# Kernel tuning notes

Hardware: AMD Instinct MI355X
Metric: run time of the kernel (lower is better)

The kernel has to match this reference:

```python
import jax, jax.numpy as jnp
import numpy as np

ROPE_THETA = 500000.0


def apply_rope(x, position_ids):
    # x: (B, H, S, hd), position_ids: (B, S)
    hd = x.shape[-1]
    inv_freq = 1.0 / (ROPE_THETA ** (jnp.arange(0, hd, 2, dtype=x.dtype) / hd))  # (hd/2,)
    freqs = position_ids.astype(x.dtype)[:, :, None] * inv_freq  # (B, S, hd/2)
    sin = jnp.sin(freqs)[:, None, :, :]  # (B, 1, S, hd/2)
    cos = jnp.cos(freqs)[:, None, :, :]
    x1 = x[..., ::2]
    x2 = x[..., 1::2]
    even = x1 * cos - x2 * sin
    odd = x2 * cos + x1 * sin
    # interleave even/odd back: stack on a new trailing axis then flatten
    return jnp.stack([even, odd], axis=-1).reshape(x.shape)


def setup_inputs() -> dict:
    key = jax.random.key(0)
    k_x, k_q, k_k, k_v, k_o = jax.random.split(key, 5)
    B, S, D = 2, 2048, 2048
    H, H_kv = 32, 8
    hd = D // H
    x = jax.random.normal(k_x, (B, S, D), dtype=jnp.float32)
    position_ids = jnp.broadcast_to(jnp.arange(S, dtype=jnp.int64)[None, :], (B, S))
    scale = 0.02
    Wq = jax.random.normal(k_q, (D, H * hd), dtype=jnp.float32) * scale
    Wk = jax.random.normal(k_k, (D, H_kv * hd), dtype=jnp.float32) * scale
    Wv = jax.random.normal(k_v, (D, H_kv * hd), dtype=jnp.float32) * scale
    Wo = jax.random.normal(k_o, (D, D), dtype=jnp.float32) * scale
    return {"x": x, "position_ids": position_ids, "Wq": Wq, "Wk": Wk, "Wv": Wv, "Wo": Wo}


def reference(x, position_ids, Wq, Wk, Wv, Wo):
    B, S, D = x.shape
    H, H_kv = 32, 8
    hd = D // H
    G = H // H_kv  # query heads per kv head

    q = (x @ Wq).reshape(B, S, H, hd).transpose(0, 2, 1, 3)        # (B, H, S, hd)
    k = (x @ Wk).reshape(B, S, H_kv, hd).transpose(0, 2, 1, 3)     # (B, H_kv, S, hd)
    v = (x @ Wv).reshape(B, S, H_kv, hd).transpose(0, 2, 1, 3)

    q = apply_rope(q, position_ids)
    k = apply_rope(k, position_ids)

    # GQA: group query heads (B, H_kv, G, S, hd); repeat_interleave maps head h -> kv head h // G
    qg = q.reshape(B, H_kv, G, S, hd)
    scores = jnp.einsum("bkgsh,bkth->bkgst", qg, k) / jnp.sqrt(jnp.asarray(hd, x.dtype))

    causal = jnp.triu(jnp.ones((S, S), dtype=bool), 1)  # True = masked
    scores = jnp.where(causal, jnp.asarray(-jnp.inf, scores.dtype), scores)

    attn = jax.nn.softmax(scores, axis=-1)  # (B, H_kv, G, S, S)
    z = jnp.einsum("bkgst,bkth->bkgsh", attn, v)  # (B, H_kv, G, S, hd)
    z = z.reshape(B, H, S, hd).transpose(0, 2, 1, 3).reshape(B, S, D)
    return z @ Wo
```

## Files before the change

### kernel.cpp

```cpp
#include <hip/hip_runtime.h>
#include <hip/hip_bf16.h>


#define S_LEN 2048
#define DIM   2048
#define NH    32
#define NKV   8
#define HD    64
#define BS    4096
#define NQKV  3072
#define LL(x) ((long long)(x))

typedef __bf16 bf16x8 __attribute__((ext_vector_type(8)));
typedef float  f32x4  __attribute__((ext_vector_type(4)));
typedef float  f32x16 __attribute__((ext_vector_type(16)));
typedef unsigned u32x4 __attribute__((ext_vector_type(4)));

__device__ __forceinline__ unsigned short bfb(float f) {
  __hip_bfloat16 h = __float2bfloat16(f);
  return *reinterpret_cast<unsigned short*>(&h);
}

__device__ __forceinline__ unsigned cvtpk(float lo, float hi) {
  unsigned u;
  asm("v_cvt_pk_bf16_f32 %0, %1, %2" : "=v"(u) : "v"(lo), "v"(hi));
  return u;
}

__device__ __forceinline__ void gload16(const void* g, void* l) {
  __builtin_amdgcn_global_load_lds(
      (const __attribute__((address_space(1))) void*)g,
      (__attribute__((address_space(3))) void*)l, 16, 0, 0);
}

__global__ void k_rope_tab(float* __restrict__ tab) {
  int i = blockIdx.x * 256 + threadIdx.x;
  if (i >= S_LEN * 32) return;
  int s = i >> 5, f = i & 31;
  double inv = pow(500000.0, -2.0 * (double)f / 64.0);
  double fr = (double)s * inv;
  tab[2 * i]     = (float)cos(fr);
  tab[2 * i + 1] = (float)sin(fr);
}

__global__ void k_cast4(const float* __restrict__ in, unsigned short* __restrict__ out, int n4) {
  int i = blockIdx.x * 256 + threadIdx.x;
  if (i >= n4) return;
  float4 v = ((const float4*)in)[i];
  ushort4 o;
  o.x = bfb(v.x); o.y = bfb(v.y); o.z = bfb(v.z); o.w = bfb(v.w);
  ((ushort4*)out)[i] = o;
}

__global__ void k_tcast(const float* __restrict__ in, unsigned short* __restrict__ out,
                        int K, int N) {
  __shared__ float tile[32][33];
  int n0 = blockIdx.x * 32, k0 = blockIdx.y * 32;
  int tx = threadIdx.x, ty = threadIdx.y;
#pragma unroll
  for (int r = 0; r < 32; r += 8) tile[ty + r][tx] = in[LL(k0 + ty + r) * N + n0 + tx];
  __syncthreads();
#pragma unroll
  for (int r = 0; r < 32; r += 8) out[LL(n0 + ty + r) * K + k0 + tx] = bfb(tile[tx][ty + r]);
}

__global__ void k_vtrans(const unsigned short* __restrict__ vbuf, unsigned short* __restrict__ vt) {
  __shared__ __align__(16) unsigned short tile[64][72];
  int s0 = blockIdx.x * 64;
  int bh = blockIdx.y;
  int b = bh >> 3, kvh = bh & 7;
  int t = threadIdx.x;
#pragma unroll
  for (int c = t; c < 512; c += 256) {
    int s = c >> 3, seg = c & 7;
    *(uint4*)&tile[s][seg * 8] =
        *(const uint4*)(vbuf + LL(b * S_LEN + s0 + s) * (NKV * HD) + kvh * HD + seg * 8);
  }
  __syncthreads();
#pragma unroll
  for (int c = t; c < 512; c += 256) {
    int d = c >> 3, sseg = c & 7;
    ushort4 x0, x1;
    unsigned short* xp = (unsigned short*)&x0;
#pragma unroll
    for (int j = 0; j < 4; j++) xp[j] = tile[sseg * 8 + j][d];
    unsigned short* yp = (unsigned short*)&x1;
#pragma unroll
    for (int j = 0; j < 4; j++) yp[j] = tile[sseg * 8 + 4 + j][d];
    uint4 o;
    o.x = ((unsigned*)&x0)[0]; o.y = ((unsigned*)&x0)[1];
    o.z = ((unsigned*)&x1)[0]; o.w = ((unsigned*)&x1)[1];
    *(uint4*)(vt + (LL(bh) * HD + d) * S_LEN + s0 + sseg * 8) = o;
  }
}

template <int MODE>
__global__ __launch_bounds__(256, 2) void k_gemm(
    const unsigned short* __restrict__ A, const unsigned short* __restrict__ Bt,
    void* __restrict__ Cout, int M, int N, int K,
    const float* __restrict__ tab, unsigned short* __restrict__ qbuf,
    unsigned short* __restrict__ kbuf, unsigned short* __restrict__ vbuf) {
  __shared__ __align__(16) unsigned short As[128 * 32];
  __shared__ __align__(16) unsigned short Bs[128 * 32];
  int t = threadIdx.x;
  int lane = t & 63, w = t >> 6;
  int wr = w >> 1, wc = w & 1;
  int g = lane >> 4, r = lane & 15;
  int gx = gridDim.x;
  int nwg = gx * gridDim.y;
  int lin = blockIdx.y * gx + blockIdx.x;
  int cpx = nwg >> 3;
  int swz = (lin & 7) * cpx + (lin >> 3);
  int bx = swz % gx, by = swz / gx;
  long long rowBase = LL(by) * 128;
  long long colBase = LL(bx) * 128;

  f32x4 acc[4][4] = {};

  int c0 = t, c1 = t + 256;
  const unsigned short* ag0 = A + (rowBase + (c0 >> 2)) * K + (c0 & 3) * 8;
  const unsigned short* ag1 = A + (rowBase + (c1 >> 2)) * K + (c1 & 3) * 8;
  const unsigned short* bg0 = Bt + (colBase + (c0 >> 2)) * K + (c0 & 3) * 8;
  const unsigned short* bg1 = Bt + (colBase + (c1 >> 2)) * K + (c1 & 3) * 8;
  char* lA0 = (char*)As + c0 * 16; char* lA1 = (char*)As + c1 * 16;
  char* lB0 = (char*)Bs + c0 * 16; char* lB1 = (char*)Bs + c1 * 16;

  for (int kt = 0; kt < K; kt += 32) {
    __syncthreads();
    gload16(ag0 + kt, lA0);
    gload16(ag1 + kt, lA1);
    gload16(bg0 + kt, lB0);
    gload16(bg1 + kt, lB1);
    __syncthreads();

    bf16x8 af[4], bfr[4];
#pragma unroll
    for (int m = 0; m < 4; m++)
      af[m] = *(const bf16x8*)(const void*)(As + (wr * 64 + m * 16 + r) * 32 + g * 8);
#pragma unroll
    for (int n = 0; n < 4; n++)
      bfr[n] = *(const bf16x8*)(const void*)(Bs + (wc * 64 + n * 16 + r) * 32 + g * 8);
#pragma unroll
    for (int m = 0; m < 4; m++)
#pragma unroll
      for (int n = 0; n < 4; n++)
        acc[m][n] = __builtin_amdgcn_mfma_f32_16x16x32_bf16(af[m], bfr[n], acc[m][n], 0, 0, 0);
  }

  if (MODE == 0) {
#pragma unroll
    for (int m = 0; m < 4; m++)
#pragma unroll
      for (int n = 0; n < 4; n++) {
        long long row0 = rowBase + wr * 64 + m * 16 + g * 4;
        long long col = colBase + wc * 64 + n * 16 + r;
#pragma unroll
        for (int j = 0; j < 4; j++)
          ((float*)Cout)[(row0 + j) * N + col] = acc[m][n][j];
      }
  } else {
#pragma unroll
    for (int n = 0; n < 4; n++) {
      int gc0 = (int)colBase + wc * 64 + n * 16;
      int gc = gc0 + r;
      unsigned short* dst; int dcol, dstride; float scale; bool rope;
      if (gc0 < 2048)      { dst = qbuf; dcol = gc;        dstride = DIM; scale = 0.18033688f; rope = true; }
      else if (gc0 < 2560) { dst = kbuf; dcol = gc - 2048; dstride = 512; scale = 1.0f;        rope = true; }
      else                 { dst = vbuf; dcol = gc - 2560; dstride = 512; scale = 1.0f;        rope = false; }
      int f = (gc & 63) >> 1;
      float sgn = (gc & 1) ? 1.f : -1.f;
#pragma unroll
      for (int m = 0; m < 4; m++) {
        long long row0 = rowBase + wr * 64 + m * 16 + g * 4;
#pragma unroll
        for (int j = 0; j < 4; j++) {
          float v = acc[m][n][j];
          float o;
          if (rope) {
            float part = __shfl_xor(v, 1);
            int s = (int)((row0 + j) & (S_LEN - 1));
            float cc = tab[(s * 32 + f) * 2], ss = tab[(s * 32 + f) * 2 + 1];
            o = (v * cc + sgn * part * ss) * scale;
          } else o = v;
          dst[(row0 + j) * dstride + dcol] = bfb(o);
        }
      }
    }
  }
}

__global__ __launch_bounds__(256, 2) void k_attn(
    const unsigned short* __restrict__ qb, const unsigned short* __restrict__ kb,
    const unsigned short* __restrict__ vt, unsigned short* __restrict__ zb) {
  int lin = blockIdx.x + 8 * (blockIdx.y + 32 * blockIdx.z);
  int kvh = lin & 7;
  int idx = lin >> 3;
  int b = idx >> 5;
  int j = idx & 31;
  int h = kvh * 4 + (j & 3);
  int pair = j >> 2;
  int bh = b * NKV + kvh;

  int t = threadIdx.x, lane = t & 63, w = t >> 6;
  int l31 = lane & 31, hi = lane >> 5;
  int sw = (l31 & 7) * 8;

  __shared__ __align__(16) unsigned short Ks[2][64 * 64];
  __shared__ __align__(16) unsigned short Vs[2][64 * 64];

  int c0 = t, c1 = t + 256;
  const unsigned short* kg0 = kb + LL(b) * S_LEN * 512 + (c0 >> 3) * 512 + kvh * HD
                                 + (((c0 & 7) ^ ((c0 >> 3) & 7)) * 8);
  const unsigned short* kg1 = kb + LL(b) * S_LEN * 512 + (c1 >> 3) * 512 + kvh * HD
                                 + (((c1 & 7) ^ ((c1 >> 3) & 7)) * 8);
  const unsigned short* vg0 = vt + (LL(bh) * HD + (c0 >> 3)) * S_LEN
                                 + (((c0 & 7) ^ ((c0 >> 3) & 7)) * 8);
  const unsigned short* vg1 = vt + (LL(bh) * HD + (c1 >> 3)) * S_LEN
                                 + (((c1 & 7) ^ ((c1 >> 3) & 7)) * 8);

#define STAGE(bufi, kst_)                                              \
  {                                                                    \
    gload16(kg0 + LL(kst_) * 512, (char*)Ks[bufi] + c0 * 16);          \
    gload16(kg1 + LL(kst_) * 512, (char*)Ks[bufi] + c1 * 16);          \
    gload16(vg0 + (kst_), (char*)Vs[bufi] + c0 * 16);                  \
    gload16(vg1 + (kst_), (char*)Vs[bufi] + c1 * 16);                  \
  }

#pragma unroll 1
  for (int pass = 0; pass < 2; pass++) {
    int st = pass ? (15 - pair) : pair;
    int rowb = st * 128 + w * 32;
    int qg = rowb + l31;
    long long qrow = LL(b) * S_LEN + qg;

    bf16x8 qf[4];
#pragma unroll
    for (int s = 0; s < 4; s++)
      qf[s] = *(const bf16x8*)(const void*)(qb + qrow * DIM + h * HD + s * 16 + hi * 8);

    f32x16 acc0 = {}, acc1 = {};
    float mrun = -1e30f, lrun = 0.f;

    int nt = 2 * st + 2;
    __syncthreads();
    STAGE(0, 0);
    for (int tt = 0; tt < nt; tt++) {
      int kst = tt * 64;
      int cur = tt & 1;
      if (tt + 1 < nt) {
        STAGE(cur ^ 1, kst + 64);
        asm volatile("s_waitcnt vmcnt(4)" ::: "memory");
      } else {
        asm volatile("s_waitcnt vmcnt(0)" ::: "memory");
      }
      __builtin_amdgcn_s_barrier();
      __builtin_amdgcn_sched_barrier(0);

      if (kst <= rowb + 31) {
        const unsigned short* Kc = Ks[cur];
        const unsigned short* Vc = Vs[cur];

        bf16x8 kf[2][4];
#pragma unroll
        for (int kbi = 0; kbi < 2; kbi++)
#pragma unroll
          for (int s = 0; s < 4; s++)
            kf[kbi][s] = *(const bf16x8*)(const void*)(
                Kc + (kbi * 32 + l31) * 64 + ((s * 16 + hi * 8) ^ sw));

        __builtin_amdgcn_s_setprio(1);
        f32x16 sc0 = {}, sc1 = {};
#pragma unroll
        for (int s = 0; s < 4; s++) {
          sc0 = __builtin_amdgcn_mfma_f32_32x32x16_bf16(kf[0][s], qf[s], sc0, 0, 0, 0);
          sc1 = __builtin_amdgcn_mfma_f32_32x32x16_bf16(kf[1][s], qf[s], sc1, 0, 0, 0);
        }
        __builtin_amdgcn_s_setprio(0);

        bf16x8 vf[8];
#pragma unroll
        for (int db = 0; db < 2; db++)
#pragma unroll
          for (int f = 0; f < 4; f++)
            vf[db * 4 + f] = *(const bf16x8*)(const void*)(
                Vc + (db * 32 + l31) * 64 + ((f * 16 + hi * 8) ^ sw));

        if (kst + 63 > rowb) {
#pragma unroll
          for (int q = 0; q < 16; q++) {
            int kl = (q & 3) + 8 * (q >> 2) + 4 * hi;
            if (kst + kl > qg) sc0[q] = -1e30f;
            if (kst + 32 + kl > qg) sc1[q] = -1e30f;
          }
        }

        float pm = -1e30f;
#pragma unroll
        for (int q = 0; q < 16; q++) {
          pm = fmaxf(pm, sc0[q]);
          pm = fmaxf(pm, sc1[q]);
        }
        pm = fmaxf(pm, __shfl_xor(pm, 32));
        if (__any(pm > mrun + 12.0f)) {
          float mnew = fmaxf(mrun, pm);
          float al = exp2f(mrun - mnew);
          mrun = mnew;
          lrun *= al;
          acc0 *= al;
          acc1 *= al;
        }
        f32x16 pv0, pv1;
        float ls = 0.f;
#pragma unroll
        for (int q = 0; q < 16; q++) {
          pv0[q] = exp2f(sc0[q] - mrun);
          pv1[q] = exp2f(sc1[q] - mrun);
          ls += pv0[q] + pv1[q];
        }
        lrun += ls + __shfl_xor(ls, 32);

        bf16x8 pfr[4];
#pragma unroll
        for (int f = 0; f < 4; f++) {
          int qb_ = (f & 1) * 8;
          float e0, e1, e2, e3, e4, e5, e6, e7;
          if (f < 2) {
            e0 = pv0[qb_ + 0]; e1 = pv0[qb_ + 1]; e2 = pv0[qb_ + 2]; e3 = pv0[qb_ + 3];
            e4 = pv0[qb_ + 4]; e5 = pv0[qb_ + 5]; e6 = pv0[qb_ + 6]; e7 = pv0[qb_ + 7];
          } else {
            e0 = pv1[qb_ + 0]; e1 = pv1[qb_ + 1]; e2 = pv1[qb_ + 2]; e3 = pv1[qb_ + 3];
            e4 = pv1[qb_ + 4]; e5 = pv1[qb_ + 5]; e6 = pv1[qb_ + 6]; e7 = pv1[qb_ + 7];
          }
          unsigned a0 = cvtpk(e0, e1), a1 = cvtpk(e2, e3);
          unsigned b0 = cvtpk(e4, e5), b1 = cvtpk(e6, e7);
          unsigned y0 = __shfl_xor(hi ? a0 : b0, 32);
          unsigned y1 = __shfl_xor(hi ? a1 : b1, 32);
          u32x4 uu;
          uu[0] = hi ? y0 : a0;
          uu[1] = hi ? y1 : a1;
          uu[2] = hi ? b0 : y0;
          uu[3] = hi ? b1 : y1;
          pfr[f] = *(bf16x8*)&uu;
        }

        __builtin_amdgcn_s_setprio(1);
#pragma unroll
        for (int f = 0; f < 4; f++) {
          acc0 = __builtin_amdgcn_mfma_f32_32x32x16_bf16(vf[f],     pfr[f], acc0, 0, 0, 0);
          acc1 = __builtin_amdgcn_mfma_f32_32x32x16_bf16(vf[4 + f], pfr[f], acc1, 0, 0, 0);
        }
        __builtin_amdgcn_s_setprio(0);
      }

      __builtin_amdgcn_sched_barrier(0);
      __builtin_amdgcn_s_barrier();
    }

    float invl = 1.0f / lrun;
#pragma unroll
    for (int q4 = 0; q4 < 4; q4++) {
      uint2 u;
      u.x = cvtpk(acc0[q4 * 4 + 0] * invl, acc0[q4 * 4 + 1] * invl);
      u.y = cvtpk(acc0[q4 * 4 + 2] * invl, acc0[q4 * 4 + 3] * invl);
      *(uint2*)(void*)(zb + qrow * DIM + h * HD + 8 * q4 + 4 * hi) = u;
      uint2 v;
      v.x = cvtpk(acc1[q4 * 4 + 0] * invl, acc1[q4 * 4 + 1] * invl);
      v.y = cvtpk(acc1[q4 * 4 + 2] * invl, acc1[q4 * 4 + 3] * invl);
      *(uint2*)(void*)(zb + qrow * DIM + h * HD + 32 + 8 * q4 + 4 * hi) = v;
    }
  }
#undef STAGE
}

extern "C" void kernel_launch(void* const* d_in, const int* in_sizes, int n_in,
                              void* d_out, int out_size, void* d_ws, size_t ws_size,
                              hipStream_t stream) {
  const float* x  = (const float*)d_in[0];
  const float* Wq = (const float*)d_in[2];
  const float* Wk = (const float*)d_in[3];
  const float* Wv = (const float*)d_in[4];
  const float* Wo = (const float*)d_in[5];
  float* out = (float*)d_out;

  char* wsb = (char*)d_ws;
  size_t off = 0;
  auto alloc = [&](size_t bytes) {
    void* p = wsb + off;
    off += (bytes + 255) & ~(size_t)255;
    return p;
  };
  float* tab            = (float*)alloc(LL(S_LEN) * 32 * 2 * 4);
  unsigned short* xb    = (unsigned short*)alloc(LL(BS) * DIM * 2);
  unsigned short* wqkvt = (unsigned short*)alloc(LL(NQKV) * DIM * 2);
  unsigned short* wot   = (unsigned short*)alloc(LL(DIM) * DIM * 2);
  unsigned short* qbuf  = (unsigned short*)alloc(LL(BS) * DIM * 2);
  unsigned short* kbuf  = (unsigned short*)alloc(LL(BS) * (NKV * HD) * 2);
  unsigned short* vbuf  = (unsigned short*)alloc(LL(BS) * (NKV * HD) * 2);
  unsigned short* vtb   = (unsigned short*)alloc(LL(2 * NKV) * HD * S_LEN * 2);
  unsigned short* zb    = (unsigned short*)alloc(LL(BS) * DIM * 2);

  k_rope_tab<<<(S_LEN * 32 + 255) / 256, 256, 0, stream>>>(tab);
  k_cast4<<<(BS * DIM / 4 + 255) / 256, 256, 0, stream>>>(x, xb, BS * DIM / 4);
  k_tcast<<<dim3(DIM / 32, DIM / 32), dim3(32, 8), 0, stream>>>(Wq, wqkvt, DIM, DIM);
  k_tcast<<<dim3(512 / 32, DIM / 32), dim3(32, 8), 0, stream>>>(Wk, wqkvt + LL(2048) * DIM, DIM, 512);
  k_tcast<<<dim3(512 / 32, DIM / 32), dim3(32, 8), 0, stream>>>(Wv, wqkvt + LL(2560) * DIM, DIM, 512);
  k_tcast<<<dim3(DIM / 32, DIM / 32), dim3(32, 8), 0, stream>>>(Wo, wot, DIM, DIM);

  k_gemm<2><<<dim3(NQKV / 128, BS / 128), 256, 0, stream>>>(
      xb, wqkvt, nullptr, BS, NQKV, DIM, tab, qbuf, kbuf, vbuf);

  k_vtrans<<<dim3(S_LEN / 64, 2 * NKV), 256, 0, stream>>>(vbuf, vtb);

  k_attn<<<dim3(8, NH, 2), 256, 0, stream>>>(qbuf, kbuf, vtb, zb);

  k_gemm<0><<<dim3(DIM / 128, BS / 128), 256, 0, stream>>>(
      zb, wot, out, BS, DIM, DIM, nullptr, nullptr, nullptr, nullptr);
}
```

Baseline: 229.8 us.

## Shrink attention blocks to two waves with 64-row query tiles

Attention blocks drop from 4 to 2 wavefronts, each covering 64 query rows, and the grid doubles so the causal work is split finer. Because every wave now needs every loaded KV tile, the per-tile skip check is removed and masking only runs on the last tile. The row max now uses v_max3 reductions and the row-sum cross-half shuffle moves out of the loop to the end. Each thread issues twice as many global-to-LDS loads per stage, and K/V tiles are reused across fewer waves, which raises load traffic per unit of compute.

```diff
diff --git a/kernel.cpp b/kernel.cpp
--- a/kernel.cpp
+++ b/kernel.cpp
@@ -25,6 +25,12 @@
   unsigned u;
   asm("v_cvt_pk_bf16_f32 %0, %1, %2" : "=v"(u) : "v"(lo), "v"(hi));
   return u;
+}
+
+__device__ __forceinline__ float fmax3(float a, float b, float c) {
+  float d;
+  asm("v_max3_f32 %0, %1, %2, %3" : "=v"(d) : "v"(a), "v"(b), "v"(c));
+  return d;
 }
 
 __device__ __forceinline__ void gload16(const void* g, void* l) {
@@ -189,14 +195,14 @@
   }
 }
 
-__global__ __launch_bounds__(256, 2) void k_attn(
+__global__ __launch_bounds__(128, 2) void k_attn(
     const unsigned short* __restrict__ qb, const unsigned short* __restrict__ kb,
     const unsigned short* __restrict__ vt, unsigned short* __restrict__ zb) {
-  int lin = blockIdx.x + 8 * (blockIdx.y + 32 * blockIdx.z);
+  int lin = blockIdx.x + 16 * (blockIdx.y + 32 * blockIdx.z);
   int kvh = lin & 7;
   int idx = lin >> 3;
-  int b = idx >> 5;
-  int j = idx & 31;
+  int b = idx >> 6;
+  int j = idx & 63;
   int h = kvh * 4 + (j & 3);
   int pair = j >> 2;
   int bh = b * NKV + kvh;
@@ -208,28 +214,34 @@
   __shared__ __align__(16) unsigned short Ks[2][64 * 64];
   __shared__ __align__(16) unsigned short Vs[2][64 * 64];
 
-  int c0 = t, c1 = t + 256;
-  const unsigned short* kg0 = kb + LL(b) * S_LEN * 512 + (c0 >> 3) * 512 + kvh * HD
-                                 + (((c0 & 7) ^ ((c0 >> 3) & 7)) * 8);
-  const unsigned short* kg1 = kb + LL(b) * S_LEN * 512 + (c1 >> 3) * 512 + kvh * HD
-                                 + (((c1 & 7) ^ ((c1 >> 3) & 7)) * 8);
-  const unsigned short* vg0 = vt + (LL(bh) * HD + (c0 >> 3)) * S_LEN
-                                 + (((c0 & 7) ^ ((c0 >> 3) & 7)) * 8);
-  const unsigned short* vg1 = vt + (LL(bh) * HD + (c1 >> 3)) * S_LEN
-                                 + (((c1 & 7) ^ ((c1 >> 3) & 7)) * 8);
+  int c0 = t, c1 = t + 128, c2 = t + 256, c3 = t + 384;
+#define KGP(c) (kb + LL(b) * S_LEN * 512 + ((c) >> 3) * 512 + kvh * HD \
+                   + ((((c) & 7) ^ (((c) >> 3) & 7)) * 8))
+#define VGP(c) (vt + (LL(bh) * HD + ((c) >> 3)) * S_LEN \
+                   + ((((c) & 7) ^ (((c) >> 3) & 7)) * 8))
+  const unsigned short* kg0 = KGP(c0); const unsigned short* kg1 = KGP(c1);
+  const unsigned short* kg2 = KGP(c2); const unsigned short* kg3 = KGP(c3);
+  const unsigned short* vg0 = VGP(c0); const unsigned short* vg1 = VGP(c1);
+  const unsigned short* vg2 = VGP(c2); const unsigned short* vg3 = VGP(c3);
+#undef KGP
+#undef VGP
 
 #define STAGE(bufi, kst_)                                              \
   {                                                                    \
     gload16(kg0 + LL(kst_) * 512, (char*)Ks[bufi] + c0 * 16);          \
     gload16(kg1 + LL(kst_) * 512, (char*)Ks[bufi] + c1 * 16);          \
+    gload16(kg2 + LL(kst_) * 512, (char*)Ks[bufi] + c2 * 16);          \
+    gload16(kg3 + LL(kst_) * 512, (char*)Ks[bufi] + c3 * 16);          \
     gload16(vg0 + (kst_), (char*)Vs[bufi] + c0 * 16);                  \
     gload16(vg1 + (kst_), (char*)Vs[bufi] + c1 * 16);                  \
+    gload16(vg2 + (kst_), (char*)Vs[bufi] + c2 * 16);                  \
+    gload16(vg3 + (kst_), (char*)Vs[bufi] + c3 * 16);                  \
   }
 
 #pragma unroll 1
   for (int pass = 0; pass < 2; pass++) {
-    int st = pass ? (15 - pair) : pair;
-    int rowb = st * 128 + w * 32;
+    int st = pass ? (31 - pair) : pair;
+    int rowb = st * 64 + w * 32;
     int qg = rowb + l31;
     long long qrow = LL(b) * S_LEN + qg;
 
@@ -241,7 +253,7 @@
     f32x16 acc0 = {}, acc1 = {};
     float mrun = -1e30f, lrun = 0.f;
 
-    int nt = 2 * st + 2;
+    int nt = st + 1;
     __syncthreads();
     STAGE(0, 0);
     for (int tt = 0; tt < nt; tt++) {
@@ -249,114 +261,125 @@
       int cur = tt & 1;
       if (tt + 1 < nt) {
         STAGE(cur ^ 1, kst + 64);
-        asm volatile("s_waitcnt vmcnt(4)" ::: "memory");
+        asm volatile("s_waitcnt vmcnt(8)" ::: "memory");
       } else {
         asm volatile("s_waitcnt vmcnt(0)" ::: "memory");
       }
       __builtin_amdgcn_s_barrier();
       __builtin_amdgcn_sched_barrier(0);
 
-      if (kst <= rowb + 31) {
-        const unsigned short* Kc = Ks[cur];
-        const unsigned short* Vc = Vs[cur];
-
-        bf16x8 kf[2][4];
-#pragma unroll
-        for (int kbi = 0; kbi < 2; kbi++)
-#pragma unroll
-          for (int s = 0; s < 4; s++)
-            kf[kbi][s] = *(const bf16x8*)(const void*)(
-                Kc + (kbi * 32 + l31) * 64 + ((s * 16 + hi * 8) ^ sw));
-
-        __builtin_amdgcn_s_setprio(1);
-        f32x16 sc0 = {}, sc1 = {};
-#pragma unroll
-        for (int s = 0; s < 4; s++) {
-          sc0 = __builtin_amdgcn_mfma_f32_32x32x16_bf16(kf[0][s], qf[s], sc0, 0, 0, 0);
-          sc1 = __builtin_amdgcn_mfma_f32_32x32x16_bf16(kf[1][s], qf[s], sc1, 0, 0, 0);
+      const unsigned short* Kc = Ks[cur];
+      const unsigned short* Vc = Vs[cur];
+
+      bf16x8 kf[2][4];
+#pragma unroll
+      for (int kbi = 0; kbi < 2; kbi++)
+#pragma unroll
+        for (int s = 0; s < 4; s++)
+          kf[kbi][s] = *(const bf16x8*)(const void*)(
+              Kc + (kbi * 32 + l31) * 64 + ((s * 16 + hi * 8) ^ sw));
+
+      __builtin_amdgcn_s_setprio(1);
+      f32x16 sc0 = {}, sc1 = {};
+#pragma unroll
+      for (int s = 0; s < 4; s++) {
+        sc0 = __builtin_amdgcn_mfma_f32_32x32x16_bf16(kf[0][s], qf[s], sc0, 0, 0, 0);
+        sc1 = __builtin_amdgcn_mfma_f32_32x32x16_bf16(kf[1][s], qf[s], sc1, 0, 0, 0);
+      }
+      __builtin_amdgcn_s_setprio(0);
+
+      bf16x8 vf[8];
+#pragma unroll
+      for (int db = 0; db < 2; db++)
+#pragma unroll
+        for (int f = 0; f < 4; f++)
+          vf[db * 4 + f] = *(const bf16x8*)(const void*)(
+              Vc + (db * 32 + l31) * 64 + ((f * 16 + hi * 8) ^ sw));
+
+      if (tt == nt - 1) {
+        int lim = qg - kst - 4 * hi;
+#pragma unroll
+        for (int q = 0; q < 16; q++) {
+          const int kl = (q & 3) + 8 * (q >> 2);
+          if (kl > lim) sc0[q] = -1e30f;
+          if (kl + 32 > lim) sc1[q] = -1e30f;
         }
-        __builtin_amdgcn_s_setprio(0);
-
-        bf16x8 vf[8];
-#pragma unroll
-        for (int db = 0; db < 2; db++)
-#pragma unroll
-          for (int f = 0; f < 4; f++)
-            vf[db * 4 + f] = *(const bf16x8*)(const void*)(
-                Vc + (db * 32 + l31) * 64 + ((f * 16 + hi * 8) ^ sw));
-
-        if (kst + 63 > rowb) {
-#pragma unroll
-          for (int q = 0; q < 16; q++) {
-            int kl = (q & 3) + 8 * (q >> 2) + 4 * hi;
-            if (kst + kl > qg) sc0[q] = -1e30f;
-            if (kst + 32 + kl > qg) sc1[q] = -1e30f;
-          }
+      }
+
+      float tq[16];
+#pragma unroll
+      for (int q = 0; q < 16; q++) tq[q] = fmaxf(sc0[q], sc1[q]);
+      float u0 = fmax3(tq[0], tq[1], tq[2]);
+      float u1 = fmax3(tq[3], tq[4], tq[5]);
+      float u2 = fmax3(tq[6], tq[7], tq[8]);
+      float u3 = fmax3(tq[9], tq[10], tq[11]);
+      float u4 = fmax3(tq[12], tq[13], tq[14]);
+      float lpm = fmaxf(fmax3(u0, u1, u2), fmax3(u3, u4, tq[15]));
+      if (__any(lpm > mrun + 12.0f)) {
+        float pmr = fmaxf(lpm, __shfl_xor(lpm, 32));
+        float mnew = fmaxf(mrun, pmr);
+        float al = exp2f(mrun - mnew);
+        mrun = mnew;
+        lrun *= al;
+        acc0 *= al;
+        acc1 *= al;
+      }
+      f32x16 pv0, pv1;
+#pragma unroll
+      for (int q = 0; q < 16; q++) {
+        pv0[q] = exp2f(sc0[q] - mrun);
+        pv1[q] = exp2f(sc1[q] - mrun);
+      }
+      {
+        float la = 0.f, lb = 0.f, lc = 0.f, ld = 0.f;
+#pragma unroll
+        for (int q = 0; q < 16; q += 4) {
+          la += pv0[q];     lb += pv0[q + 1];
+          lc += pv0[q + 2]; ld += pv0[q + 3];
+          la += pv1[q];     lb += pv1[q + 1];
+          lc += pv1[q + 2]; ld += pv1[q + 3];
         }
-
-        float pm = -1e30f;
-#pragma unroll
-        for (int q = 0; q < 16; q++) {
-          pm = fmaxf(pm, sc0[q]);
-          pm = fmaxf(pm, sc1[q]);
+        lrun += (la + lb) + (lc + ld);
+      }
+
+      bf16x8 pfr[4];
+#pragma unroll
+      for (int f = 0; f < 4; f++) {
+        int qb_ = (f & 1) * 8;
+        float e0, e1, e2, e3, e4, e5, e6, e7;
+        if (f < 2) {
+          e0 = pv0[qb_ + 0]; e1 = pv0[qb_ + 1]; e2 = pv0[qb_ + 2]; e3 = pv0[qb_ + 3];
+          e4 = pv0[qb_ + 4]; e5 = pv0[qb_ + 5]; e6 = pv0[qb_ + 6]; e7 = pv0[qb_ + 7];
+        } else {
+          e0 = pv1[qb_ + 0]; e1 = pv1[qb_ + 1]; e2 = pv1[qb_ + 2]; e3 = pv1[qb_ + 3];
+          e4 = pv1[qb_ + 4]; e5 = pv1[qb_ + 5]; e6 = pv1[qb_ + 6]; e7 = pv1[qb_ + 7];
         }
-        pm = fmaxf(pm, __shfl_xor(pm, 32));
-        if (__any(pm > mrun + 12.0f)) {
-          float mnew = fmaxf(mrun, pm);
-          float al = exp2f(mrun - mnew);
-          mrun = mnew;
-          lrun *= al;
-          acc0 *= al;
-          acc1 *= al;
-        }
-        f32x16 pv0, pv1;
-        float ls = 0.f;
-#pragma unroll
-        for (int q = 0; q < 16; q++) {
-          pv0[q] = exp2f(sc0[q] - mrun);
-          pv1[q] = exp2f(sc1[q] - mrun);
-          ls += pv0[q] + pv1[q];
-        }
-        lrun += ls + __shfl_xor(ls, 32);
-
-        bf16x8 pfr[4];
-#pragma unroll
-        for (int f = 0; f < 4; f++) {
-          int qb_ = (f & 1) * 8;
-          float e0, e1, e2, e3, e4, e5, e6, e7;
-          if (f < 2) {
-            e0 = pv0[qb_ + 0]; e1 = pv0[qb_ + 1]; e2 = pv0[qb_ + 2]; e3 = pv0[qb_ + 3];
-            e4 = pv0[qb_ + 4]; e5 = pv0[qb_ + 5]; e6 = pv0[qb_ + 6]; e7 = pv0[qb_ + 7];
-          } else {
-            e0 = pv1[qb_ + 0]; e1 = pv1[qb_ + 1]; e2 = pv1[qb_ + 2]; e3 = pv1[qb_ + 3];
-            e4 = pv1[qb_ + 4]; e5 = pv1[qb_ + 5]; e6 = pv1[qb_ + 6]; e7 = pv1[qb_ + 7];
-          }
-          unsigned a0 = cvtpk(e0, e1), a1 = cvtpk(e2, e3);
-          unsigned b0 = cvtpk(e4, e5), b1 = cvtpk(e6, e7);
-          unsigned y0 = __shfl_xor(hi ? a0 : b0, 32);
-          unsigned y1 = __shfl_xor(hi ? a1 : b1, 32);
-          u32x4 uu;
-          uu[0] = hi ? y0 : a0;
-          uu[1] = hi ? y1 : a1;
-          uu[2] = hi ? b0 : y0;
-          uu[3] = hi ? b1 : y1;
-          pfr[f] = *(bf16x8*)&uu;
-        }
-
-        __builtin_amdgcn_s_setprio(1);
-#pragma unroll
-        for (int f = 0; f < 4; f++) {
-          acc0 = __builtin_amdgcn_mfma_f32_32x32x16_bf16(vf[f],     pfr[f], acc0, 0, 0, 0);
-          acc1 = __builtin_amdgcn_mfma_f32_32x32x16_bf16(vf[4 + f], pfr[f], acc1, 0, 0, 0);
-        }
-        __builtin_amdgcn_s_setprio(0);
-      }
+        unsigned a0 = cvtpk(e0, e1), a1 = cvtpk(e2, e3);
+        unsigned b0 = cvtpk(e4, e5), b1 = cvtpk(e6, e7);
+        unsigned y0 = __shfl_xor(hi ? a0 : b0, 32);
+        unsigned y1 = __shfl_xor(hi ? a1 : b1, 32);
+        u32x4 uu;
+        uu[0] = hi ? y0 : a0;
+        uu[1] = hi ? y1 : a1;
+        uu[2] = hi ? b0 : y0;
+        uu[3] = hi ? b1 : y1;
+        pfr[f] = *(bf16x8*)&uu;
+      }
+
+      __builtin_amdgcn_s_setprio(1);
+#pragma unroll
+      for (int f = 0; f < 4; f++) {
+        acc0 = __builtin_amdgcn_mfma_f32_32x32x16_bf16(vf[f],     pfr[f], acc0, 0, 0, 0);
+        acc1 = __builtin_amdgcn_mfma_f32_32x32x16_bf16(vf[4 + f], pfr[f], acc1, 0, 0, 0);
+      }
+      __builtin_amdgcn_s_setprio(0);
 
       __builtin_amdgcn_sched_barrier(0);
       __builtin_amdgcn_s_barrier();
     }
 
-    float invl = 1.0f / lrun;
+    float lfull = lrun + __shfl_xor(lrun, 32);
+    float invl = 1.0f / lfull;
 #pragma unroll
     for (int q4 = 0; q4 < 4; q4++) {
       uint2 u;
@@ -411,7 +434,7 @@
 
   k_vtrans<<<dim3(S_LEN / 64, 2 * NKV), 256, 0, stream>>>(vbuf, vtb);
 
-  k_attn<<<dim3(8, NH, 2), 256, 0, stream>>>(qbuf, kbuf, vtb, zb);
+  k_attn<<<dim3(16, NH, 2), 128, 0, stream>>>(qbuf, kbuf, vtb, zb);
 
   k_gemm<0><<<dim3(DIM / 128, BS / 128), 256, 0, stream>>>(
       zb, wot, out, BS, DIM, DIM, nullptr, nullptr, nullptr, nullptr);
```

New measurement: 232.7 us. Within noise of the previous version (+1.3%).

## Fuse prep kernels into one launch and streamline softmax reductions

Applied to the files above, without the earlier changes.

Merges the rope table, x cast, and four weight transpose-cast kernels into one launch whose block-index ranges dispatch to each job, removing five kernel launches and their gaps. In the attention inner loop, the row max now uses v_max3 and the cross-half shuffle runs only when a rescale is needed. The running denominator is kept per half-wave and summed with a single shuffle at the end. These trim per-iteration ALU and shuffle work in the softmax. The prep kernel is correct only if its hard-coded block ranges keep matching the tensor sizes.

```diff
diff --git a/kernel.cpp b/kernel.cpp
--- a/kernel.cpp
+++ b/kernel.cpp
@@ -27,41 +27,66 @@
   return u;
 }
 
+__device__ __forceinline__ float fmax3(float a, float b, float c) {
+  float d;
+  asm("v_max3_f32 %0, %1, %2, %3" : "=v"(d) : "v"(a), "v"(b), "v"(c));
+  return d;
+}
+
 __device__ __forceinline__ void gload16(const void* g, void* l) {
   __builtin_amdgcn_global_load_lds(
       (const __attribute__((address_space(1))) void*)g,
       (__attribute__((address_space(3))) void*)l, 16, 0, 0);
 }
 
-__global__ void k_rope_tab(float* __restrict__ tab) {
-  int i = blockIdx.x * 256 + threadIdx.x;
-  if (i >= S_LEN * 32) return;
-  int s = i >> 5, f = i & 31;
-  double inv = pow(500000.0, -2.0 * (double)f / 64.0);
-  double fr = (double)s * inv;
-  tab[2 * i]     = (float)cos(fr);
-  tab[2 * i + 1] = (float)sin(fr);
-}
-
-__global__ void k_cast4(const float* __restrict__ in, unsigned short* __restrict__ out, int n4) {
-  int i = blockIdx.x * 256 + threadIdx.x;
-  if (i >= n4) return;
-  float4 v = ((const float4*)in)[i];
-  ushort4 o;
-  o.x = bfb(v.x); o.y = bfb(v.y); o.z = bfb(v.z); o.w = bfb(v.w);
-  ((ushort4*)out)[i] = o;
-}
-
-__global__ void k_tcast(const float* __restrict__ in, unsigned short* __restrict__ out,
-                        int K, int N) {
-  __shared__ float tile[32][33];
-  int n0 = blockIdx.x * 32, k0 = blockIdx.y * 32;
-  int tx = threadIdx.x, ty = threadIdx.y;
-#pragma unroll
-  for (int r = 0; r < 32; r += 8) tile[ty + r][tx] = in[LL(k0 + ty + r) * N + n0 + tx];
+__device__ __forceinline__ void tcast_body(
+    const float* __restrict__ in, unsigned short* __restrict__ out,
+    int K, int N, int bx, int by, int tid, float* tile ) {
+  int n0 = bx * 32, k0 = by * 32;
+  int tx = tid & 31, ty = tid >> 5;
+#pragma unroll
+  for (int r = 0; r < 32; r += 8)
+    tile[(ty + r) * 33 + tx] = in[LL(k0 + ty + r) * N + n0 + tx];
   __syncthreads();
 #pragma unroll
-  for (int r = 0; r < 32; r += 8) out[LL(n0 + ty + r) * K + k0 + tx] = bfb(tile[tx][ty + r]);
+  for (int r = 0; r < 32; r += 8)
+    out[LL(n0 + ty + r) * K + k0 + tx] = bfb(tile[tx * 33 + ty + r]);
+}
+
+__global__ __launch_bounds__(256) void k_prep(
+    const float* __restrict__ x,  const float* __restrict__ Wq,
+    const float* __restrict__ Wk, const float* __restrict__ Wv,
+    const float* __restrict__ Wo, float* __restrict__ tab,
+    unsigned short* __restrict__ xb, unsigned short* __restrict__ wqkvt,
+    unsigned short* __restrict__ wot) {
+  __shared__ float tile[32 * 33];
+  int blk = blockIdx.x, tid = threadIdx.x;
+  if (blk < 256) {
+    int i = blk * 256 + tid;
+    int s = i >> 5, f = i & 31;
+    double inv = pow(500000.0, -2.0 * (double)f / 64.0);
+    double fr = (double)s * inv;
+    tab[2 * i]     = (float)cos(fr);
+    tab[2 * i + 1] = (float)sin(fr);
+  } else if (blk < 8448) {
+    int i = (blk - 256) * 256 + tid;
+    float4 v = ((const float4*)x)[i];
+    ushort4 o;
+    o.x = bfb(v.x); o.y = bfb(v.y); o.z = bfb(v.z); o.w = bfb(v.w);
+    ((ushort4*)xb)[i] = o;
+  } else if (blk < 12544) {
+    int t2 = blk - 8448;
+    tcast_body(Wq, wqkvt, DIM, DIM, t2 & 63, t2 >> 6, tid, tile);
+  } else if (blk < 13568) {
+    int t3 = blk - 12544;
+    tcast_body(Wk, wqkvt + LL(2048) * DIM, DIM, 512, t3 & 15, t3 >> 4, tid, tile);
+  } else if (blk < 14592) {
+    int t4 = blk - 13568;
+    tcast_body(Wv, wqkvt + LL(2560) * DIM, DIM, 512, t4 & 15, t4 >> 4, tid, tile);
+  } else {
+    int t5 = blk - 14592;
+    tcast_body(Wo, wot, DIM, DIM, t5 & 63, t5 >> 6, tid, tile);
+  }
 }
 
 __global__ void k_vtrans(const unsigned short* __restrict__ vbuf, unsigned short* __restrict__ vt) {
@@ -294,15 +319,18 @@
           }
         }
 
-        float pm = -1e30f;
-#pragma unroll
-        for (int q = 0; q < 16; q++) {
-          pm = fmaxf(pm, sc0[q]);
-          pm = fmaxf(pm, sc1[q]);
-        }
-        pm = fmaxf(pm, __shfl_xor(pm, 32));
-        if (__any(pm > mrun + 12.0f)) {
-          float mnew = fmaxf(mrun, pm);
+        float tq[16];
+#pragma unroll
+        for (int q = 0; q < 16; q++) tq[q] = fmaxf(sc0[q], sc1[q]);
+        float u0 = fmax3(tq[0], tq[1], tq[2]);
+        float u1 = fmax3(tq[3], tq[4], tq[5]);
+        float u2 = fmax3(tq[6], tq[7], tq[8]);
+        float u3 = fmax3(tq[9], tq[10], tq[11]);
+        float u4 = fmax3(tq[12], tq[13], tq[14]);
+        float lpm = fmaxf(fmax3(u0, u1, u2), fmax3(u3, u4, tq[15]));
+        if (__any(lpm > mrun + 12.0f)) {
+          float pmr = fmaxf(lpm, __shfl_xor(lpm, 32));
+          float mnew = fmaxf(mrun, pmr);
           float al = exp2f(mrun - mnew);
           mrun = mnew;
           lrun *= al;
@@ -310,14 +338,22 @@
           acc1 *= al;
         }
         f32x16 pv0, pv1;
-        float ls = 0.f;
 #pragma unroll
         for (int q = 0; q < 16; q++) {
           pv0[q] = exp2f(sc0[q] - mrun);
           pv1[q] = exp2f(sc1[q] - mrun);
-          ls += pv0[q] + pv1[q];
-        }
-        lrun += ls + __shfl_xor(ls, 32);
+        }
+        {
+          float la = 0.f, lb = 0.f, lc = 0.f, ld = 0.f;
+#pragma unroll
+          for (int q = 0; q < 16; q += 4) {
+            la += pv0[q];     lb += pv0[q + 1];
+            lc += pv0[q + 2]; ld += pv0[q + 3];
+            la += pv1[q];     lb += pv1[q + 1];
+            lc += pv1[q + 2]; ld += pv1[q + 3];
+          }
+          lrun += (la + lb) + (lc + ld);
+        }
 
         bf16x8 pfr[4];
 #pragma unroll
@@ -356,7 +392,8 @@
       __builtin_amdgcn_s_barrier();
     }
 
-    float invl = 1.0f / lrun;
+    float lfull = lrun + __shfl_xor(lrun, 32);
+    float invl = 1.0f / lfull;
 #pragma unroll
     for (int q4 = 0; q4 < 4; q4++) {
       uint2 u;
@@ -399,12 +436,7 @@
   unsigned short* vtb   = (unsigned short*)alloc(LL(2 * NKV) * HD * S_LEN * 2);
   unsigned short* zb    = (unsigned short*)alloc(LL(BS) * DIM * 2);
 
-  k_rope_tab<<<(S_LEN * 32 + 255) / 256, 256, 0, stream>>>(tab);
-  k_cast4<<<(BS * DIM / 4 + 255) / 256, 256, 0, stream>>>(x, xb, BS * DIM / 4);
-  k_tcast<<<dim3(DIM / 32, DIM / 32), dim3(32, 8), 0, stream>>>(Wq, wqkvt, DIM, DIM);
-  k_tcast<<<dim3(512 / 32, DIM / 32), dim3(32, 8), 0, stream>>>(Wk, wqkvt + LL(2048) * DIM, DIM, 512);
-  k_tcast<<<dim3(512 / 32, DIM / 32), dim3(32, 8), 0, stream>>>(Wv, wqkvt + LL(2560) * DIM, DIM, 512);
-  k_tcast<<<dim3(DIM / 32, DIM / 32), dim3(32, 8), 0, stream>>>(Wo, wot, DIM, DIM);
+  k_prep<<<18688, 256, 0, stream>>>(x, Wq, Wk, Wv, Wo, tab, xb, wqkvt, wot);
 
   k_gemm<2><<<dim3(NQKV / 128, BS / 128), 256, 0, stream>>>(
       xb, wqkvt, nullptr, BS, NQKV, DIM, tab, qbuf, kbuf, vbuf);
```

Measured after the change: 221.8 us. 3.4% less time.
